# Kernel tuning notes

Measured on AMD Instinct MI355X. Metric: run time of the kernel, lower is better.

## Reference

```python
import jax, jax.numpy as jnp
import numpy as np

N = 100000


def _gcn_conv(x, edge_index, W, b):
    # GCNConv with add_self_loops=True, symmetric normalization.
    src, dst = edge_index[0], edge_index[1]
    loop = jnp.arange(N, dtype=src.dtype)
    src = jnp.concatenate([src, loop])
    dst = jnp.concatenate([dst, loop])
    # degree of target nodes (edge weights all 1, incl. self loops)
    deg = jax.ops.segment_sum(jnp.ones_like(dst, dtype=x.dtype), dst, num_segments=N)
    dinv = jnp.where(deg > 0, jax.lax.rsqrt(deg), 0.0)
    norm = dinv[src] * dinv[dst]  # [E+N]
    h = x @ W  # [N, out]
    msg = h[src] * norm[:, None]  # gather + scale, [E+N, out]
    out = jax.ops.segment_sum(msg, dst, num_segments=N)  # scatter-add
    return out + b


def setup_inputs() -> dict:
    key = jax.random.key(0)
    k1, k2, k3, k4 = jax.random.split(key, 4)
    input_dim, hidden, output_dim = 256, 64, 128
    E = 1600000
    x = jax.random.normal(k1, (N, input_dim), dtype=jnp.float32)
    edge_index = jax.random.randint(k2, (2, E), 0, N, dtype=jnp.int64)
    W1 = jax.random.normal(k3, (input_dim, hidden), dtype=jnp.float32) / np.sqrt(input_dim)
    b1 = jnp.zeros((hidden,), dtype=jnp.float32)
    W2 = jax.random.normal(k4, (hidden, output_dim), dtype=jnp.float32) / np.sqrt(hidden)
    b2 = jnp.zeros((output_dim,), dtype=jnp.float32)
    return {"x": x, "edge_index": edge_index, "W1": W1, "b1": b1, "W2": W2, "b2": b2}


def reference(x, edge_index, W1, b1, W2, b2):
    h = jax.nn.relu(_gcn_conv(x, edge_index, W1, b1))
    return _gcn_conv(h, edge_index, W2, b2)
```

## Files before the change

### kernel.cpp

```cpp
#include <hip/hip_runtime.h>
#include <hip/hip_fp16.h>

#define NNODES 100000
#define NBUCK 391
#define NB_CHUNK 256
#define NC (NBUCK * NB_CHUNK)
#define SCAN_ELEMS 1024

typedef _Float16 f16x8 __attribute__((ext_vector_type(8)));
typedef float    f32x4 __attribute__((ext_vector_type(4)));

__global__ void detect_kernel(const int* __restrict__ raw, int* __restrict__ flag) {
    __shared__ int cnt;
    if (threadIdx.x == 0) cnt = 0;
    __syncthreads();
    if (threadIdx.x < 100) {
        if (raw[2 * threadIdx.x + 1] == 0) atomicAdd(&cnt, 1);
    }
    __syncthreads();
    if (threadIdx.x == 0) *flag = (cnt > 50) ? 1 : 0;
}

__global__ __launch_bounds__(256) void count_kernel(const int* __restrict__ raw,
                                                    int* __restrict__ counts,
                                                    int E, int CE, const int* __restrict__ flag) {
    __shared__ int hist[NBUCK];
    for (int i = threadIdx.x; i < NBUCK; i += 256) hist[i] = 0;
    __syncthreads();
    int b = blockIdx.x;
    int isI64 = *flag;
    int beg = b * CE;
    int end = beg + CE; if (end > E) end = E;
    for (int e = beg + (int)threadIdx.x; e < end; e += 256) {
        int d = isI64 ? raw[2 * E + 2 * e] : raw[E + e];
        atomicAdd(&hist[d >> 8], 1);
    }
    __syncthreads();
    for (int k = threadIdx.x; k < NBUCK; k += 256)
        counts[k * NB_CHUNK + b] = hist[k];
}

__global__ __launch_bounds__(256) void scan_partial_kernel(const int* __restrict__ in,
                                                           int* __restrict__ bsum, int n) {
    int base = blockIdx.x * SCAN_ELEMS + threadIdx.x * 4;
    int s = 0;
    if (base + 3 < n) {
        int4 v = *reinterpret_cast<const int4*>(&in[base]);
        s = v.x + v.y + v.z + v.w;
    } else {
        for (int i = base; i < n && i < base + 4; ++i) s += in[i];
    }
#pragma unroll
    for (int d = 32; d; d >>= 1) s += __shfl_down(s, d, 64);
    __shared__ int ws[4];
    int wid = threadIdx.x >> 6;
    if ((threadIdx.x & 63) == 0) ws[wid] = s;
    __syncthreads();
    if (threadIdx.x == 0) bsum[blockIdx.x] = ws[0] + ws[1] + ws[2] + ws[3];
}

__global__ void scan_partials_kernel(const int* __restrict__ bsum, int* __restrict__ boff,
                                     int* __restrict__ total_out, int nb) {
    __shared__ int s[128];
    int t = threadIdx.x;
    s[t] = (t < nb) ? bsum[t] : 0;
    __syncthreads();
    for (int d = 1; d < 128; d <<= 1) {
        int v = (t >= d) ? s[t - d] : 0;
        __syncthreads();
        s[t] += v;
        __syncthreads();
    }
    if (t < nb) boff[t] = (t == 0) ? 0 : s[t - 1];
    if (t == 127) *total_out = s[127];
}

__global__ __launch_bounds__(256) void scan_write_kernel(const int* __restrict__ in,
                                                         const int* __restrict__ boff,
                                                         int* __restrict__ outp, int n) {
    __shared__ int ts[256];
    int base = blockIdx.x * SCAN_ELEMS + threadIdx.x * 4;
    int v0 = 0, v1 = 0, v2 = 0, v3 = 0;
    if (base + 3 < n) {
        int4 v = *reinterpret_cast<const int4*>(&in[base]);
        v0 = v.x; v1 = v.y; v2 = v.z; v3 = v.w;
    } else {
        if (base < n)     v0 = in[base];
        if (base + 1 < n) v1 = in[base + 1];
        if (base + 2 < n) v2 = in[base + 2];
    }
    ts[threadIdx.x] = v0 + v1 + v2 + v3;
    __syncthreads();
    for (int d = 1; d < 256; d <<= 1) {
        int t = (threadIdx.x >= d) ? ts[threadIdx.x - d] : 0;
        __syncthreads();
        ts[threadIdx.x] += t;
        __syncthreads();
    }
    int run = boff[blockIdx.x] + ((threadIdx.x == 0) ? 0 : ts[threadIdx.x - 1]);
    if (base < n)     { outp[base] = run;     run += v0; }
    if (base + 1 < n) { outp[base + 1] = run; run += v1; }
    if (base + 2 < n) { outp[base + 2] = run; run += v2; }
    if (base + 3 < n) { outp[base + 3] = run; }
}

__global__ __launch_bounds__(256) void scatter_kernel(const int* __restrict__ raw,
                                                      const int* __restrict__ cbase,
                                                      int* __restrict__ cw,
                                                      int E, int CE, const int* __restrict__ flag) {
    __shared__ int cur[NBUCK];
    int b = blockIdx.x;
    for (int k = threadIdx.x; k < NBUCK; k += 256)
        cur[k] = cbase[k * NB_CHUNK + b];
    __syncthreads();
    int isI64 = *flag;
    int beg = b * CE;
    int end = beg + CE; if (end > E) end = E;
    for (int e = beg + (int)threadIdx.x; e < end; e += 256) {
        int s, d;
        if (isI64) { s = raw[2 * e]; d = raw[2 * E + 2 * e]; }
        else       { s = raw[e];     d = raw[E + e]; }
        int pos = atomicAdd(&cur[d >> 8], 1);
        cw[pos] = s | ((d & 255) << 24);
    }
}

__global__ __launch_bounds__(256) void histdeg_kernel(const int* __restrict__ cw,
                                                      const int* __restrict__ cbase,
                                                      int* __restrict__ indeg,
                                                      float* __restrict__ dinv, int n) {
    __shared__ int hist[256];
    hist[threadIdx.x] = 0;
    __syncthreads();
    int k = blockIdx.x;
    int beg = cbase[k * NB_CHUNK];
    int end = cbase[(k + 1) * NB_CHUNK];
    for (int e = beg + (int)threadIdx.x; e < end; e += 256)
        atomicAdd(&hist[(cw[e] >> 24) & 255], 1);
    __syncthreads();
    int i = (k << 8) + threadIdx.x;
    if (i < n) {
        int dg = hist[threadIdx.x];
        indeg[i] = dg;
        dinv[i] = rsqrtf((float)(dg + 1));
    }
}

__global__ __launch_bounds__(256) void fillcol_kernel(const int* __restrict__ cw,
                                                      const int* __restrict__ cbase,
                                                      const int* __restrict__ ptr,
                                                      int* __restrict__ col, int n) {
    __shared__ int cur[256];
    int k = blockIdx.x;
    int i = (k << 8) + threadIdx.x;
    cur[threadIdx.x] = (i < n) ? ptr[i] : 0;
    __syncthreads();
    int beg = cbase[k * NB_CHUNK];
    int end = cbase[(k + 1) * NB_CHUNK];
    for (int e = beg + (int)threadIdx.x; e < end; e += 256) {
        int v = cw[e];
        int pos = atomicAdd(&cur[(v >> 24) & 255], 1);
        col[pos] = v & 0x00FFFFFF;
    }
}

__global__ void wfrag_kernel(const float* __restrict__ W, __half* __restrict__ wf) {
    int flat = blockIdx.x * 256 + threadIdx.x;
    int j  = flat & 7;
    int l  = (flat >> 3) & 63;
    int nb = (flat >> 9) & 3;
    int kc = flat >> 11;
    int k  = kc * 32 + ((l >> 4) << 3) + j;
    int nc = nb * 16 + (l & 15);
    wf[flat] = __float2half(W[k * 64 + nc]);
}

__global__ __launch_bounds__(256) void gemm1_kernel(const float* __restrict__ x,
                                                    const __half* __restrict__ wf,
                                                    __half* __restrict__ H, int M) {
    __shared__ __half xs[64][264];
    int tid = threadIdx.x;
    int bm = blockIdx.x * 64;
    const float4* x4 = reinterpret_cast<const float4*>(x);
#pragma unroll
    for (int i = 0; i < 16; ++i) {
        int lin = i * 256 + tid;
        int row = lin >> 6;
        int c4  = lin & 63;
        int gr = bm + row; if (gr >= M) gr = M - 1;
        float4 v = x4[(size_t)gr * 64 + c4];
        __half* dst = &xs[row][c4 * 4];
        dst[0] = __float2half(v.x); dst[1] = __float2half(v.y);
        dst[2] = __float2half(v.z); dst[3] = __float2half(v.w);
    }
    __syncthreads();
    int w = tid >> 6;
    int l = tid & 63;
    int lrow = l & 15;
    int lk   = l >> 4;
    const f16x8* wf8 = reinterpret_cast<const f16x8*>(wf);
    f32x4 acc[4] = {};
#pragma unroll
    for (int kc = 0; kc < 8; ++kc) {
        f16x8 a = *reinterpret_cast<const f16x8*>(&xs[w * 16 + lrow][kc * 32 + lk * 8]);
#pragma unroll
        for (int nb = 0; nb < 4; ++nb) {
            f16x8 b = wf8[(kc * 4 + nb) * 64 + l];
            acc[nb] = __builtin_amdgcn_mfma_f32_16x16x32_f16(a, b, acc[nb], 0, 0, 0);
        }
    }
#pragma unroll
    for (int nb = 0; nb < 4; ++nb)
#pragma unroll
        for (int r = 0; r < 4; ++r) {
            int row = bm + w * 16 + lk * 4 + r;
            if (row < M) H[(size_t)row * 64 + nb * 16 + lrow] = __float2half(acc[nb][r]);
        }
}

__global__ __launch_bounds__(256) void aggregate_kernel(const __half* __restrict__ h,
                                                        const int* __restrict__ ptr,
                                                        const int* __restrict__ col,
                                                        const float* __restrict__ dinv,
                                                        const float* __restrict__ bias,
                                                        void* __restrict__ out, int n,
                                                        int relu, int out_half) {
    int node = (blockIdx.x << 2) + (threadIdx.x >> 6);
    if (node >= n) return;
    int lane = threadIdx.x & 63;
    int g  = lane >> 3;
    int fl = (lane & 7) << 3;
    float acc[8] = {};
    int pend = ptr[node + 1];
    int p = ptr[node] + g;
    for (; p + 8 < pend; p += 16) {
        int c0 = col[p];
        int c1 = col[p + 8];
        uint4 r0 = *reinterpret_cast<const uint4*>(&h[(size_t)c0 * 64 + fl]);
        uint4 r1 = *reinterpret_cast<const uint4*>(&h[(size_t)c1 * 64 + fl]);
        float w0 = dinv[c0], w1 = dinv[c1];
        const unsigned* u0 = &r0.x;
        const unsigned* u1 = &r1.x;
#pragma unroll
        for (int k = 0; k < 4; ++k) {
            float2 f0 = __half22float2(*reinterpret_cast<const __half2*>(&u0[k]));
            float2 f1 = __half22float2(*reinterpret_cast<const __half2*>(&u1[k]));
            acc[2 * k]     = fmaf(w0, f0.x, acc[2 * k]);
            acc[2 * k + 1] = fmaf(w0, f0.y, acc[2 * k + 1]);
            acc[2 * k]     = fmaf(w1, f1.x, acc[2 * k]);
            acc[2 * k + 1] = fmaf(w1, f1.y, acc[2 * k + 1]);
        }
    }
    if (p < pend) {
        int c0 = col[p];
        uint4 r0 = *reinterpret_cast<const uint4*>(&h[(size_t)c0 * 64 + fl]);
        float w0 = dinv[c0];
        const unsigned* u0 = &r0.x;
#pragma unroll
        for (int k = 0; k < 4; ++k) {
            float2 f0 = __half22float2(*reinterpret_cast<const __half2*>(&u0[k]));
            acc[2 * k]     = fmaf(w0, f0.x, acc[2 * k]);
            acc[2 * k + 1] = fmaf(w0, f0.y, acc[2 * k + 1]);
        }
    }
#pragma unroll
    for (int j = 0; j < 8; ++j) {
        acc[j] += __shfl_xor(acc[j], 8, 64);
        acc[j] += __shfl_xor(acc[j], 16, 64);
        acc[j] += __shfl_xor(acc[j], 32, 64);
    }
    if (g == 0) {
        float di = dinv[node];
        uint4 sv = *reinterpret_cast<const uint4*>(&h[(size_t)node * 64 + fl]);
        const unsigned* su = &sv.x;
        float v[8];
#pragma unroll
        for (int k = 0; k < 4; ++k) {
            float2 f = __half22float2(*reinterpret_cast<const __half2*>(&su[k]));
            v[2 * k]     = fmaf(di, f.x, acc[2 * k]) * di;
            v[2 * k + 1] = fmaf(di, f.y, acc[2 * k + 1]) * di;
        }
        if (bias) {
            float4 b0 = *reinterpret_cast<const float4*>(&bias[fl]);
            float4 b1 = *reinterpret_cast<const float4*>(&bias[fl + 4]);
            v[0] += b0.x; v[1] += b0.y; v[2] += b0.z; v[3] += b0.w;
            v[4] += b1.x; v[5] += b1.y; v[6] += b1.z; v[7] += b1.w;
        }
        if (relu) {
#pragma unroll
            for (int j = 0; j < 8; ++j) v[j] = fmaxf(v[j], 0.f);
        }
        if (out_half) {
            __half hv[8];
#pragma unroll
            for (int j = 0; j < 8; ++j) hv[j] = __float2half(v[j]);
            *reinterpret_cast<uint4*>(&((__half*)out)[(size_t)node * 64 + fl]) =
                *reinterpret_cast<const uint4*>(hv);
        } else {
            float* fo = (float*)out;
            *reinterpret_cast<float4*>(&fo[(size_t)node * 64 + fl]) =
                make_float4(v[0], v[1], v[2], v[3]);
            *reinterpret_cast<float4*>(&fo[(size_t)node * 64 + fl + 4]) =
                make_float4(v[4], v[5], v[6], v[7]);
        }
    }
}

__global__ __launch_bounds__(256) void gemm2_kernel(const float* __restrict__ A,
                                                    const float* __restrict__ W,
                                                    const float* __restrict__ bias,
                                                    float* __restrict__ out, int M) {
    __shared__ float as[64][65];
    __shared__ float ws[64][128];
    int tid = threadIdx.x;
    int bm = blockIdx.x * 64;
    int ty = tid >> 4, tx = tid & 15;
#pragma unroll
    for (int i = 0; i < 4; ++i) {
        int lin = (tid << 2) + i;
        int r = lin >> 4;
        int c = (lin & 15) << 2;
        float4 v = make_float4(0.f, 0.f, 0.f, 0.f);
        int gr = bm + r;
        if (gr < M) v = *reinterpret_cast<const float4*>(&A[(size_t)gr * 64 + c]);
        as[r][c] = v.x; as[r][c + 1] = v.y; as[r][c + 2] = v.z; as[r][c + 3] = v.w;
    }
#pragma unroll
    for (int i = 0; i < 8; ++i) {
        int lin = tid + (i << 8);
        int r = lin >> 5;
        int c = (lin & 31) << 2;
        *reinterpret_cast<float4*>(&ws[r][c]) =
            *reinterpret_cast<const float4*>(&W[(size_t)r * 128 + c]);
    }
    __syncthreads();
    float acc[4][8] = {};
#pragma unroll 8
    for (int kk = 0; kk < 64; ++kk) {
        float a[4];
#pragma unroll
        for (int i = 0; i < 4; ++i) a[i] = as[ty * 4 + i][kk];
        float b[8];
        float4 b0 = *reinterpret_cast<const float4*>(&ws[kk][tx * 8]);
        float4 b1 = *reinterpret_cast<const float4*>(&ws[kk][tx * 8 + 4]);
        b[0] = b0.x; b[1] = b0.y; b[2] = b0.z; b[3] = b0.w;
        b[4] = b1.x; b[5] = b1.y; b[6] = b1.z; b[7] = b1.w;
#pragma unroll
        for (int i = 0; i < 4; ++i)
#pragma unroll
            for (int j = 0; j < 8; ++j)
                acc[i][j] = fmaf(a[i], b[j], acc[i][j]);
    }
#pragma unroll
    for (int i = 0; i < 4; ++i) {
        int gr = bm + ty * 4 + i;
        if (gr >= M) continue;
#pragma unroll
        for (int jv = 0; jv < 2; ++jv) {
            int cbase = tx * 8 + jv * 4;
            float4 o;
            o.x = acc[i][jv * 4 + 0] + bias[cbase + 0];
            o.y = acc[i][jv * 4 + 1] + bias[cbase + 1];
            o.z = acc[i][jv * 4 + 2] + bias[cbase + 2];
            o.w = acc[i][jv * 4 + 3] + bias[cbase + 3];
            *reinterpret_cast<float4*>(&out[(size_t)gr * 128 + cbase]) = o;
        }
    }
}

extern "C" void kernel_launch(void* const* d_in, const int* in_sizes, int n_in,
                              void* d_out, int out_size, void* d_ws, size_t ws_size,
                              hipStream_t stream) {
    const float* x  = (const float*)d_in[0];
    const int*   ei = (const int*)d_in[1];
    const float* W1 = (const float*)d_in[2];
    const float* b1 = (const float*)d_in[3];
    const float* W2 = (const float*)d_in[4];
    const float* b2 = (const float*)d_in[5];
    float* out = (float*)d_out;
    const int n = NNODES;
    const int E = in_sizes[1] / 2;
    const int CE = (E + NB_CHUNK - 1) / NB_CHUNK;

    char* w = (char*)d_ws;
    auto alloc = [&](size_t bytes) {
        char* p = w;
        w += (bytes + 255) & ~(size_t)255;
        return p;
    };
    int*    flag   = (int*)   alloc(4);
    int*    counts = (int*)   alloc((size_t)NC * 4);
    int*    cbase  = (int*)   alloc((size_t)(NC + 1) * 4);
    int*    indeg  = (int*)   alloc((size_t)n * 4);
    float*  dinv   = (float*) alloc((size_t)n * 4);
    int*    ptr    = (int*)   alloc((size_t)(n + 1) * 4);
    int*    bsum   = (int*)   alloc(128 * 4);
    int*    boff   = (int*)   alloc(128 * 4);
    int*    cw     = (int*)   alloc((size_t)E * 4);
    int*    col    = (int*)   alloc((size_t)E * 4);
    __half* wfrag  = (__half*)alloc(16384 * 2);
    __half* H1     = (__half*)alloc((size_t)n * 64 * 2);
    __half* h1     = (__half*)alloc((size_t)n * 64 * 2);
    float*  A2     = (float*) alloc((size_t)n * 64 * 4);

    int sbC = (NC + SCAN_ELEMS - 1) / SCAN_ELEMS;
    int sbN = (n  + SCAN_ELEMS - 1) / SCAN_ELEMS;

    detect_kernel<<<1, 128, 0, stream>>>(ei, flag);
    wfrag_kernel<<<64, 256, 0, stream>>>(W1, wfrag);
    count_kernel<<<NB_CHUNK, 256, 0, stream>>>(ei, counts, E, CE, flag);
    scan_partial_kernel<<<sbC, 256, 0, stream>>>(counts, bsum, NC);
    scan_partials_kernel<<<1, 128, 0, stream>>>(bsum, boff, &cbase[NC], sbC);
    scan_write_kernel<<<sbC, 256, 0, stream>>>(counts, boff, cbase, NC);
    scatter_kernel<<<NB_CHUNK, 256, 0, stream>>>(ei, cbase, cw, E, CE, flag);
    histdeg_kernel<<<NBUCK, 256, 0, stream>>>(cw, cbase, indeg, dinv, n);
    scan_partial_kernel<<<sbN, 256, 0, stream>>>(indeg, bsum, n);
    scan_partials_kernel<<<1, 128, 0, stream>>>(bsum, boff, &ptr[n], sbN);
    scan_write_kernel<<<sbN, 256, 0, stream>>>(indeg, boff, ptr, n);
    fillcol_kernel<<<NBUCK, 256, 0, stream>>>(cw, cbase, ptr, col, n);

    gemm1_kernel<<<(n + 63) / 64, 256, 0, stream>>>(x, wfrag, H1, n);
    aggregate_kernel<<<(n + 3) / 4, 256, 0, stream>>>(H1, ptr, col, dinv, b1, h1, n, 1, 1);
    aggregate_kernel<<<(n + 3) / 4, 256, 0, stream>>>(h1, ptr, col, dinv, nullptr, A2, n, 0, 0);
    gemm2_kernel<<<(n + 63) / 64, 256, 0, stream>>>(A2, W2, b2, out, n);
}
```

Measured before the change: 207.9 us.

## Use MFMA fp16 for second GEMM, fp16 aggregate output, compact edge indices

Replaces the fp32 shared-memory second GEMM with an MFMA 16x16x32 fp16 kernel that reads a pre-swizzled W2 fragment buffer. The second aggregation now writes half-precision output, halving its write and GEMM read traffic. The edge-count pass also writes 32-bit src/dst copies so the scatter pass reads compact arrays instead of strided int64 data. This adds precision loss in the second layer input and an extra write of the edge arrays.

Measured after the change: 198.2 us. -4.7%, faster.

```diff
diff --git a/kernel.cpp b/kernel.cpp
--- a/kernel.cpp
+++ b/kernel.cpp
@@ -21,9 +21,12 @@
     if (threadIdx.x == 0) *flag = (cnt > 50) ? 1 : 0;
 }
 
-__global__ __launch_bounds__(256) void count_kernel(const int* __restrict__ raw,
-                                                    int* __restrict__ counts,
-                                                    int E, int CE, const int* __restrict__ flag) {
+__global__ __launch_bounds__(256) void convert_count_kernel(const int* __restrict__ raw,
+                                                            int* __restrict__ src32,
+                                                            int* __restrict__ dst32,
+                                                            int* __restrict__ counts,
+                                                            int E, int CE,
+                                                            const int* __restrict__ flag) {
     __shared__ int hist[NBUCK];
     for (int i = threadIdx.x; i < NBUCK; i += 256) hist[i] = 0;
     __syncthreads();
@@ -32,7 +35,11 @@
     int beg = b * CE;
     int end = beg + CE; if (end > E) end = E;
     for (int e = beg + (int)threadIdx.x; e < end; e += 256) {
-        int d = isI64 ? raw[2 * E + 2 * e] : raw[E + e];
+        int s, d;
+        if (isI64) { s = raw[2 * e]; d = raw[2 * E + 2 * e]; }
+        else       { s = raw[e];     d = raw[E + e]; }
+        src32[e] = s;
+        dst32[e] = d;
         atomicAdd(&hist[d >> 8], 1);
     }
     __syncthreads();
@@ -104,22 +111,21 @@
     if (base + 3 < n) { outp[base + 3] = run; }
 }
 
-__global__ __launch_bounds__(256) void scatter_kernel(const int* __restrict__ raw,
+__global__ __launch_bounds__(256) void scatter_kernel(const int* __restrict__ src32,
+                                                      const int* __restrict__ dst32,
                                                       const int* __restrict__ cbase,
                                                       int* __restrict__ cw,
-                                                      int E, int CE, const int* __restrict__ flag) {
+                                                      int E, int CE) {
     __shared__ int cur[NBUCK];
     int b = blockIdx.x;
     for (int k = threadIdx.x; k < NBUCK; k += 256)
         cur[k] = cbase[k * NB_CHUNK + b];
     __syncthreads();
-    int isI64 = *flag;
     int beg = b * CE;
     int end = beg + CE; if (end > E) end = E;
     for (int e = beg + (int)threadIdx.x; e < end; e += 256) {
-        int s, d;
-        if (isI64) { s = raw[2 * e]; d = raw[2 * E + 2 * e]; }
-        else       { s = raw[e];     d = raw[E + e]; }
+        int s = src32[e];
+        int d = dst32[e];
         int pos = atomicAdd(&cur[d >> 8], 1);
         cw[pos] = s | ((d & 255) << 24);
     }
@@ -173,6 +179,17 @@
     int k  = kc * 32 + ((l >> 4) << 3) + j;
     int nc = nb * 16 + (l & 15);
     wf[flat] = __float2half(W[k * 64 + nc]);
+}
+
+__global__ void wfrag2_kernel(const float* __restrict__ W, __half* __restrict__ wf) {
+    int flat = blockIdx.x * 256 + threadIdx.x;
+    int j  = flat & 7;
+    int l  = (flat >> 3) & 63;
+    int nb = (flat >> 9) & 7;
+    int kc = flat >> 12;
+    int k  = kc * 32 + ((l >> 4) << 3) + j;
+    int nc = nb * 16 + (l & 15);
+    wf[flat] = __float2half(W[k * 128 + nc]);
 }
 
 __global__ __launch_bounds__(256) void gemm1_kernel(const float* __restrict__ x,
@@ -306,64 +323,33 @@
     }
 }
 
-__global__ __launch_bounds__(256) void gemm2_kernel(const float* __restrict__ A,
-                                                    const float* __restrict__ W,
+__global__ __launch_bounds__(256) void gemm2_kernel(const __half* __restrict__ A,
+                                                    const __half* __restrict__ wf,
                                                     const float* __restrict__ bias,
                                                     float* __restrict__ out, int M) {
-    __shared__ float as[64][65];
-    __shared__ float ws[64][128];
     int tid = threadIdx.x;
-    int bm = blockIdx.x * 64;
-    int ty = tid >> 4, tx = tid & 15;
-#pragma unroll
-    for (int i = 0; i < 4; ++i) {
-        int lin = (tid << 2) + i;
-        int r = lin >> 4;
-        int c = (lin & 15) << 2;
-        float4 v = make_float4(0.f, 0.f, 0.f, 0.f);
-        int gr = bm + r;
-        if (gr < M) v = *reinterpret_cast<const float4*>(&A[(size_t)gr * 64 + c]);
-        as[r][c] = v.x; as[r][c + 1] = v.y; as[r][c + 2] = v.z; as[r][c + 3] = v.w;
-    }
-#pragma unroll
-    for (int i = 0; i < 8; ++i) {
-        int lin = tid + (i << 8);
-        int r = lin >> 5;
-        int c = (lin & 31) << 2;
-        *reinterpret_cast<float4*>(&ws[r][c]) =
-            *reinterpret_cast<const float4*>(&W[(size_t)r * 128 + c]);
-    }
-    __syncthreads();
-    float acc[4][8] = {};
-#pragma unroll 8
-    for (int kk = 0; kk < 64; ++kk) {
-        float a[4];
-#pragma unroll
-        for (int i = 0; i < 4; ++i) a[i] = as[ty * 4 + i][kk];
-        float b[8];
-        float4 b0 = *reinterpret_cast<const float4*>(&ws[kk][tx * 8]);
-        float4 b1 = *reinterpret_cast<const float4*>(&ws[kk][tx * 8 + 4]);
-        b[0] = b0.x; b[1] = b0.y; b[2] = b0.z; b[3] = b0.w;
-        b[4] = b1.x; b[5] = b1.y; b[6] = b1.z; b[7] = b1.w;
-#pragma unroll
-        for (int i = 0; i < 4; ++i)
-#pragma unroll
-            for (int j = 0; j < 8; ++j)
-                acc[i][j] = fmaf(a[i], b[j], acc[i][j]);
-    }
-#pragma unroll
-    for (int i = 0; i < 4; ++i) {
-        int gr = bm + ty * 4 + i;
-        if (gr >= M) continue;
-#pragma unroll
-        for (int jv = 0; jv < 2; ++jv) {
-            int cbase = tx * 8 + jv * 4;
-            float4 o;
-            o.x = acc[i][jv * 4 + 0] + bias[cbase + 0];
-            o.y = acc[i][jv * 4 + 1] + bias[cbase + 1];
-            o.z = acc[i][jv * 4 + 2] + bias[cbase + 2];
-            o.w = acc[i][jv * 4 + 3] + bias[cbase + 3];
-            *reinterpret_cast<float4*>(&out[(size_t)gr * 128 + cbase]) = o;
+    int w = tid >> 6;
+    int l = tid & 63;
+    int lrow = l & 15;
+    int lk   = l >> 4;
+    int base = blockIdx.x * 64 + w * 16;
+    int arow = base + lrow; if (arow >= M) arow = M - 1;
+    f16x8 a0 = *reinterpret_cast<const f16x8*>(&A[(size_t)arow * 64 + lk * 8]);
+    f16x8 a1 = *reinterpret_cast<const f16x8*>(&A[(size_t)arow * 64 + 32 + lk * 8]);
+    const f16x8* wf8 = reinterpret_cast<const f16x8*>(wf);
+    f32x4 acc[8] = {};
+#pragma unroll
+    for (int nb = 0; nb < 8; ++nb) {
+        acc[nb] = __builtin_amdgcn_mfma_f32_16x16x32_f16(a0, wf8[nb * 64 + l], acc[nb], 0, 0, 0);
+        acc[nb] = __builtin_amdgcn_mfma_f32_16x16x32_f16(a1, wf8[(8 + nb) * 64 + l], acc[nb], 0, 0, 0);
+    }
+#pragma unroll
+    for (int nb = 0; nb < 8; ++nb) {
+        float bv = bias[nb * 16 + lrow];
+#pragma unroll
+        for (int r = 0; r < 4; ++r) {
+            int row = base + lk * 4 + r;
+            if (row < M) out[(size_t)row * 128 + nb * 16 + lrow] = acc[nb][r] + bv;
         }
     }
 }
@@ -389,6 +375,8 @@
         return p;
     };
     int*    flag   = (int*)   alloc(4);
+    int*    src32  = (int*)   alloc((size_t)E * 4);
+    int*    dst32  = (int*)   alloc((size_t)E * 4);
     int*    counts = (int*)   alloc((size_t)NC * 4);
     int*    cbase  = (int*)   alloc((size_t)(NC + 1) * 4);
     int*    indeg  = (int*)   alloc((size_t)n * 4);
@@ -399,20 +387,22 @@
     int*    cw     = (int*)   alloc((size_t)E * 4);
     int*    col    = (int*)   alloc((size_t)E * 4);
     __half* wfrag  = (__half*)alloc(16384 * 2);
+    __half* wfrag2 = (__half*)alloc(8192 * 2);
     __half* H1     = (__half*)alloc((size_t)n * 64 * 2);
     __half* h1     = (__half*)alloc((size_t)n * 64 * 2);
-    float*  A2     = (float*) alloc((size_t)n * 64 * 4);
+    __half* A2     = (__half*)alloc((size_t)n * 64 * 2);
 
     int sbC = (NC + SCAN_ELEMS - 1) / SCAN_ELEMS;
     int sbN = (n  + SCAN_ELEMS - 1) / SCAN_ELEMS;
 
     detect_kernel<<<1, 128, 0, stream>>>(ei, flag);
     wfrag_kernel<<<64, 256, 0, stream>>>(W1, wfrag);
-    count_kernel<<<NB_CHUNK, 256, 0, stream>>>(ei, counts, E, CE, flag);
+    wfrag2_kernel<<<32, 256, 0, stream>>>(W2, wfrag2);
+    convert_count_kernel<<<NB_CHUNK, 256, 0, stream>>>(ei, src32, dst32, counts, E, CE, flag);
     scan_partial_kernel<<<sbC, 256, 0, stream>>>(counts, bsum, NC);
     scan_partials_kernel<<<1, 128, 0, stream>>>(bsum, boff, &cbase[NC], sbC);
     scan_write_kernel<<<sbC, 256, 0, stream>>>(counts, boff, cbase, NC);
-    scatter_kernel<<<NB_CHUNK, 256, 0, stream>>>(ei, cbase, cw, E, CE, flag);
+    scatter_kernel<<<NB_CHUNK, 256, 0, stream>>>(src32, dst32, cbase, cw, E, CE);
     histdeg_kernel<<<NBUCK, 256, 0, stream>>>(cw, cbase, indeg, dinv, n);
     scan_partial_kernel<<<sbN, 256, 0, stream>>>(indeg, bsum, n);
     scan_partials_kernel<<<1, 128, 0, stream>>>(bsum, boff, &ptr[n], sbN);
@@ -421,6 +411,6 @@
 
     gemm1_kernel<<<(n + 63) / 64, 256, 0, stream>>>(x, wfrag, H1, n);
     aggregate_kernel<<<(n + 3) / 4, 256, 0, stream>>>(H1, ptr, col, dinv, b1, h1, n, 1, 1);
-    aggregate_kernel<<<(n + 3) / 4, 256, 0, stream>>>(h1, ptr, col, dinv, nullptr, A2, n, 0, 0);
-    gemm2_kernel<<<(n + 63) / 64, 256, 0, stream>>>(A2, W2, b2, out, n);
-}
+    aggregate_kernel<<<(n + 3) / 4, 256, 0, stream>>>(h1, ptr, col, dinv, nullptr, A2, n, 0, 1);
+    gemm2_kernel<<<(n + 63) / 64, 256, 0, stream>>>(A2, wfrag2, b2, out, n);
+}
```
